# Performance work log

Hardware: AMD Instinct MI355X
Metric: run time of the kernel (lower is better)

The kernel has to match this reference:

```python
import jax, jax.numpy as jnp
import numpy as np

N_HEADS = 16
DIM = 1024
NEG_INF = -1e20  # neginf for fp32 per original module


def setup_inputs() -> dict:
    key = jax.random.key(0)
    ks = jax.random.split(key, 10)
    B, N, D = 2, 2048, DIM
    std = np.sqrt(2.0 / (D + D))  # xavier_normal for square weights
    inp = {
        "query": jax.random.normal(ks[0], (B, N, D), dtype=jnp.float32),
        "mask": jax.random.randint(ks[1], (B, N), 0, 2, dtype=jnp.int32),
        "wq": jax.random.normal(ks[2], (D, D), dtype=jnp.float32) * std,
        "bq": jnp.zeros((D,), dtype=jnp.float32),
        "wk": jax.random.normal(ks[3], (D, D), dtype=jnp.float32) * std,
        "bk": jnp.zeros((D,), dtype=jnp.float32),
        "wv": jax.random.normal(ks[4], (D, D), dtype=jnp.float32) * std,
        "bv": jnp.zeros((D,), dtype=jnp.float32),
        "wo": jax.random.normal(ks[5], (D, D), dtype=jnp.float32) * std,
        "bo": jnp.zeros((D,), dtype=jnp.float32),
    }
    return inp


def reference(query, mask, wq, bq, wk, bk, wv, bv, wo, bo):
    B, N, D = query.shape
    H = N_HEADS
    dh = D // H
    scale = jnp.asarray(np.sqrt(dh), dtype=query.dtype)

    def heads(x):  # [B,N,D] -> [B,H,N,dh]
        return x.reshape(B, N, H, dh).transpose(0, 2, 1, 3)

    q = heads(query @ wq.T + bq) / scale
    k = heads(query @ wk.T + bk)
    v = heads(query @ wv.T + bv)

    # [B,H,Nq,Nk] scaled dot-product scores, masked where mask==0
    dot_prod = jnp.einsum("bhqd,bhkd->bhqk", q, k)
    dot_prod = jnp.where(mask[:, None, None, :] == 0, NEG_INF, dot_prod)

    attn = jax.nn.softmax(dot_prod.astype(jnp.float32), axis=-1).astype(query.dtype)
    # dropout p=0 -> identity
    ctx = jnp.einsum("bhqk,bhkd->bhqd", attn, v)
    ctx = ctx.transpose(0, 2, 1, 3).reshape(B, N, D)
    out = ctx @ wo.T + bo
    # original returns dot_prod as [B*H, Nq, Nk]
    return out, dot_prod.reshape(B * H, N, N)
```

## Files before the change

### kernel.cpp

```cpp
#include <hip/hip_runtime.h>

typedef unsigned short u16;
typedef __attribute__((ext_vector_type(8))) __bf16 bf16x8;
typedef __attribute__((ext_vector_type(4))) float f32x4;

#define MFMA(a, b, c) __builtin_amdgcn_mfma_f32_16x16x32_bf16((a), (b), (c), 0, 0, 0)

__device__ __forceinline__ u16 f2bf(float f) {
  union { float f; unsigned u; } v; v.f = f;
  unsigned r = v.u + 0x7fffu + ((v.u >> 16) & 1u);
  return (u16)(r >> 16);
}

__device__ __forceinline__ void gld16(const u16* g, u16* l) {
  __builtin_amdgcn_global_load_lds(
      (const __attribute__((address_space(1))) unsigned int*)(g),
      (__attribute__((address_space(3))) unsigned int*)(l), 16, 0, 0);
}

__global__ __launch_bounds__(256) void k_cast(
    const float* __restrict__ query, const float* __restrict__ wq,
    const float* __restrict__ wk, const float* __restrict__ wv,
    const float* __restrict__ wo, u16* __restrict__ dst)
{
  size_t i = ((size_t)blockIdx.x * 256 + threadIdx.x) * 8;
  const float* src; size_t off; float sc = 1.0f;
  if (i < 4194304u)      { src = query; off = i; }
  else if (i < 5242880u) { src = wq; off = i - 4194304u; sc = 0.125f; }
  else if (i < 6291456u) { src = wk; off = i - 5242880u; }
  else if (i < 7340032u) { src = wv; off = i - 6291456u; }
  else                   { src = wo; off = i - 7340032u; }
  float4 a = *(const float4*)(src + off);
  float4 b = *(const float4*)(src + off + 4);
  alignas(16) u16 r[8] = { f2bf(a.x*sc), f2bf(a.y*sc), f2bf(a.z*sc), f2bf(a.w*sc),
                           f2bf(b.x*sc), f2bf(b.y*sc), f2bf(b.z*sc), f2bf(b.w*sc) };
  *(int4*)(dst + i) = *(int4*)r;
}

__global__ __launch_bounds__(256) void k_gemm_qkv(
    const u16* __restrict__ Ab, const u16* __restrict__ Wb,
    const float* __restrict__ bq, const float* __restrict__ bk, const float* __restrict__ bv,
    u16* __restrict__ Qh, u16* __restrict__ Kh, u16* __restrict__ Vh)
{
  const int fb = blockIdx.x;
  const int sb = (fb & 7) * 96 + (fb >> 3);
  const int n0 = (sb % 24) * 128;
  const int m0 = (sb / 24) * 128;
  const int tid = threadIdx.x;
  const int w = tid >> 6, lane = tid & 63, g = lane >> 4, l15 = lane & 15;
  const int wm = w >> 1, wn = w & 1;
  __shared__ alignas(16) u16 As[128 * 32];
  __shared__ alignas(16) u16 Bs[128 * 32];
  f32x4 acc[4][4] = {};
  for (int k0 = 0; k0 < 1024; k0 += 32) {
    __syncthreads();
#pragma unroll
    for (int t = 0; t < 2; ++t) {
      int i = t * 256 + tid;
      int row = i >> 2, ch = i & 3, sch = ch ^ (row & 3);
      gld16(Ab + (size_t)(m0 + row) * 1024 + k0 + sch * 8, As + i * 8);
    }
#pragma unroll
    for (int t = 0; t < 2; ++t) {
      int i = t * 256 + tid;
      int row = i >> 2, ch = i & 3, sch = ch ^ (row & 3);
      gld16(Wb + (size_t)(n0 + row) * 1024 + k0 + sch * 8, Bs + i * 8);
    }
    __syncthreads();
    bf16x8 af[4], bfr[4];
#pragma unroll
    for (int i = 0; i < 4; ++i) {
      int row = wm * 64 + i * 16 + l15;
      af[i] = *(const bf16x8*)(As + (row * 4 + (g ^ (row & 3))) * 8);
    }
#pragma unroll
    for (int j = 0; j < 4; ++j) {
      int row = wn * 64 + j * 16 + l15;
      bfr[j] = *(const bf16x8*)(Bs + (row * 4 + (g ^ (row & 3))) * 8);
    }
#pragma unroll
    for (int i = 0; i < 4; ++i)
#pragma unroll
      for (int j = 0; j < 4; ++j)
        acc[i][j] = MFMA(af[i], bfr[j], acc[i][j]);
  }
  const int proj = n0 >> 10;
  const float* bias = (proj == 0) ? bq : (proj == 1) ? bk : bv;
  const float bsc = (proj == 0) ? 0.125f : 1.0f;
  u16* dst = (proj == 0) ? Qh : (proj == 1) ? Kh : Vh;
#pragma unroll
  for (int i = 0; i < 4; ++i)
#pragma unroll
    for (int j = 0; j < 4; ++j)
#pragma unroll
      for (int jj = 0; jj < 4; ++jj) {
        int mr = m0 + wm * 64 + i * 16 + g * 4 + jj;
        int c  = n0 + wn * 64 + j * 16 + l15;
        int d = c & 1023, h = d >> 6, d64 = d & 63;
        int b = mr >> 11, n = mr & 2047;
        float v = acc[i][j][jj] + bias[d] * bsc;
        dst[((size_t)((b << 4) | h) * 2048 + n) * 64 + d64] = f2bf(v);
      }
}

__global__ __launch_bounds__(256) void k_gemm_out(
    const u16* __restrict__ Ab, const u16* __restrict__ Wb,
    const float* __restrict__ bo, float* __restrict__ out)
{
  const int fb = blockIdx.x;
  const int sb = (fb & 7) * 32 + (fb >> 3);
  const int n0 = (sb & 7) * 128;
  const int m0 = (sb >> 3) * 128;
  const int tid = threadIdx.x;
  const int w = tid >> 6, lane = tid & 63, g = lane >> 4, l15 = lane & 15;
  const int wm = w >> 1, wn = w & 1;
  __shared__ alignas(16) u16 As[128 * 32];
  __shared__ alignas(16) u16 Bs[128 * 32];
  f32x4 acc[4][4] = {};
  for (int k0 = 0; k0 < 1024; k0 += 32) {
    __syncthreads();
#pragma unroll
    for (int t = 0; t < 2; ++t) {
      int i = t * 256 + tid;
      int row = i >> 2, ch = i & 3, sch = ch ^ (row & 3);
      gld16(Ab + (size_t)(m0 + row) * 1024 + k0 + sch * 8, As + i * 8);
    }
#pragma unroll
    for (int t = 0; t < 2; ++t) {
      int i = t * 256 + tid;
      int row = i >> 2, ch = i & 3, sch = ch ^ (row & 3);
      gld16(Wb + (size_t)(n0 + row) * 1024 + k0 + sch * 8, Bs + i * 8);
    }
    __syncthreads();
    bf16x8 af[4], bfr[4];
#pragma unroll
    for (int i = 0; i < 4; ++i) {
      int row = wm * 64 + i * 16 + l15;
      af[i] = *(const bf16x8*)(As + (row * 4 + (g ^ (row & 3))) * 8);
    }
#pragma unroll
    for (int j = 0; j < 4; ++j) {
      int row = wn * 64 + j * 16 + l15;
      bfr[j] = *(const bf16x8*)(Bs + (row * 4 + (g ^ (row & 3))) * 8);
    }
#pragma unroll
    for (int i = 0; i < 4; ++i)
#pragma unroll
      for (int j = 0; j < 4; ++j)
        acc[i][j] = MFMA(af[i], bfr[j], acc[i][j]);
  }
#pragma unroll
  for (int i = 0; i < 4; ++i)
#pragma unroll
    for (int j = 0; j < 4; ++j)
#pragma unroll
      for (int jj = 0; jj < 4; ++jj) {
        int mr = m0 + wm * 64 + i * 16 + g * 4 + jj;
        int c  = n0 + wn * 64 + j * 16 + l15;
        out[(size_t)mr * 1024 + c] = acc[i][j][jj] + bo[c];
      }
}

__global__ __launch_bounds__(256) void k_transpose_v(
    const u16* __restrict__ Vh, u16* __restrict__ Vt)
{
  const int n0 = blockIdx.x * 64;
  const int bh = blockIdx.y;
  const int tid = threadIdx.x;
  __shared__ alignas(16) u16 t[64][72];
  const u16* src = Vh + ((size_t)bh * 2048 + n0) * 64;
#pragma unroll
  for (int it = 0; it < 2; ++it) {
    int i = it * 256 + tid;
    int row = i >> 3, c = (i & 7) * 8;
    *(int4*)(&t[row][c]) = *(const int4*)(src + i * 8);
  }
  __syncthreads();
#pragma unroll
  for (int it = 0; it < 2; ++it) {
    int i = it * 256 + tid;
    int d = i >> 3, nn = (i & 7) * 8;
    alignas(16) u16 tmp[8];
#pragma unroll
    for (int e = 0; e < 8; ++e) tmp[e] = t[nn + e][d];
    *(int4*)(Vt + ((size_t)bh * 64 + d) * 2048 + n0 + nn) = *(int4*)tmp;
  }
}

__global__ __launch_bounds__(256) void k_attn(
    const u16* __restrict__ Qh, const u16* __restrict__ Kh, const u16* __restrict__ Vt,
    const int* __restrict__ mask, float* __restrict__ dout, u16* __restrict__ ctx)
{
  const int fb = blockIdx.x;
  const int sb = (fb & 7) * 128 + (fb >> 3);
  const int qt = sb & 31;
  const int bh = sb >> 5;
  const int b  = bh >> 4;
  const int tid = threadIdx.x;
  const int w = tid >> 6, lane = tid & 63, g = lane >> 4, l15 = lane & 15;
  __shared__ alignas(16) u16 Ks[128 * 64];
  __shared__ alignas(16) u16 Vs[64 * 128];
  __shared__ alignas(16) u16 Ps[4][16 * 136];

  const u16* Qrow = Qh + ((size_t)bh * 2048 + qt * 64 + w * 16 + l15) * 64;
  bf16x8 qf[2];
  qf[0] = *(const bf16x8*)(Qrow + g * 8);
  qf[1] = *(const bf16x8*)(Qrow + 32 + g * 8);

  float m[4] = {-3e38f, -3e38f, -3e38f, -3e38f};
  float l[4] = {0.f, 0.f, 0.f, 0.f};
  f32x4 O[4] = {};
  const int* maskb = mask + b * 2048;
  float* Sbase = dout + 4194304 + (size_t)bh * 4194304
               + (size_t)(qt * 64 + w * 16 + g * 4) * 2048 + l15;

  for (int kt = 0; kt < 16; ++kt) {
    __syncthreads();
    const u16* Kg = Kh + ((size_t)bh * 2048 + kt * 128) * 64;
#pragma unroll
    for (int it = 0; it < 4; ++it) {
      int i = it * 256 + tid;
      int row = i >> 3, ch = i & 7, sch = ch ^ (row & 7);
      gld16(Kg + row * 64 + sch * 8, Ks + i * 8);
    }
    const u16* Vg = Vt + (size_t)bh * 131072 + kt * 128;
#pragma unroll
    for (int it = 0; it < 4; ++it) {
      int i = it * 256 + tid;
      int row = i >> 4, ch = i & 15, sch = ch ^ (row & 15);
      gld16(Vg + (size_t)row * 2048 + sch * 8, Vs + i * 8);
    }
    int mk[8];
#pragma unroll
    for (int f = 0; f < 8; ++f) mk[f] = maskb[kt * 128 + f * 16 + l15];
    __syncthreads();

    f32x4 s[8];
#pragma unroll
    for (int f = 0; f < 8; ++f) {
      int row = f * 16 + l15;
      bf16x8 kf0 = *(const bf16x8*)(Ks + (row * 8 + ((0 + g) ^ (row & 7))) * 8);
      bf16x8 kf1 = *(const bf16x8*)(Ks + (row * 8 + ((4 + g) ^ (row & 7))) * 8);
      f32x4 t = {};
      t = MFMA(qf[0], kf0, t);
      t = MFMA(qf[1], kf1, t);
      s[f] = t;
    }

    float fb8[8];
#pragma unroll
    for (int f = 0; f < 8; ++f) fb8[f] = (mk[f] != 0) ? 0.f : -1e20f;

    float mloc[4] = {-3e38f, -3e38f, -3e38f, -3e38f};
#pragma unroll
    for (int jj = 0; jj < 4; ++jj)
#pragma unroll
      for (int f = 0; f < 8; ++f) {
        float sv = s[f][jj] + fb8[f];
        s[f][jj] = sv;
        __builtin_nontemporal_store(sv, &Sbase[(size_t)jj * 2048 + kt * 128 + f * 16]);
        mloc[jj] = fmaxf(mloc[jj], sv);
      }
#pragma unroll
    for (int d = 1; d < 16; d <<= 1)
#pragma unroll
      for (int jj = 0; jj < 4; ++jj)
        mloc[jj] = fmaxf(mloc[jj], __shfl_xor(mloc[jj], d, 64));

    float corr[4];
#pragma unroll
    for (int jj = 0; jj < 4; ++jj) {
      float mn = fmaxf(m[jj], mloc[jj]);
      corr[jj] = __expf(m[jj] - mn);
      m[jj] = mn;
    }
    float psum[4] = {0.f, 0.f, 0.f, 0.f};
#pragma unroll
    for (int f = 0; f < 8; ++f)
#pragma unroll
      for (int jj = 0; jj < 4; ++jj) {
        float p = __expf(s[f][jj] - m[jj]);
        psum[jj] += p;
        Ps[w][(g * 4 + jj) * 136 + f * 16 + l15] = f2bf(p);
      }
#pragma unroll
    for (int d = 1; d < 16; d <<= 1)
#pragma unroll
      for (int jj = 0; jj < 4; ++jj)
        psum[jj] += __shfl_xor(psum[jj], d, 64);
#pragma unroll
    for (int jj = 0; jj < 4; ++jj) l[jj] = l[jj] * corr[jj] + psum[jj];
#pragma unroll
    for (int fd = 0; fd < 4; ++fd)
#pragma unroll
      for (int jj = 0; jj < 4; ++jj) O[fd][jj] *= corr[jj];

#pragma unroll
    for (int fk = 0; fk < 4; ++fk) {
      bf16x8 pa = *(const bf16x8*)(&Ps[w][l15 * 136 + fk * 32 + g * 8]);
#pragma unroll
      for (int fd = 0; fd < 4; ++fd) {
        int row = fd * 16 + l15;
        bf16x8 bv = *(const bf16x8*)(Vs + (row * 16 + ((fk * 4 + g) ^ (row & 15))) * 8);
        O[fd] = MFMA(pa, bv, O[fd]);
      }
    }
  }
  float inv[4];
#pragma unroll
  for (int jj = 0; jj < 4; ++jj) inv[jj] = 1.0f / l[jj];
  const int h = bh & 15;
#pragma unroll
  for (int fd = 0; fd < 4; ++fd)
#pragma unroll
    for (int jj = 0; jj < 4; ++jj) {
      int n = qt * 64 + w * 16 + g * 4 + jj;
      int c = h * 64 + fd * 16 + l15;
      ctx[((size_t)(b * 2048 + n)) * 1024 + c] = f2bf(O[fd][jj] * inv[jj]);
    }
}

extern "C" void kernel_launch(void* const* d_in, const int* in_sizes, int n_in,
                              void* d_out, int out_size, void* d_ws, size_t ws_size,
                              hipStream_t stream)
{
  const float* query = (const float*)d_in[0];
  const int*   mask  = (const int*)d_in[1];
  const float* wq = (const float*)d_in[2];
  const float* bq = (const float*)d_in[3];
  const float* wk = (const float*)d_in[4];
  const float* bk = (const float*)d_in[5];
  const float* wv = (const float*)d_in[6];
  const float* bv = (const float*)d_in[7];
  const float* wo = (const float*)d_in[8];
  const float* bo = (const float*)d_in[9];
  float* out = (float*)d_out;

  u16* ws   = (u16*)d_ws;
  u16* Ab   = ws;
  u16* Wqkv = ws + 4194304;
  u16* Wo   = ws + 7340032;
  u16* Qh   = ws + 8388608;
  u16* Kh   = ws + 12582912;
  u16* Vh   = ws + 16777216;
  u16* Vt   = ws + 20971520;
  u16* ctx  = ws + 25165824;

  k_cast<<<4096, 256, 0, stream>>>(query, wq, wk, wv, wo, ws);
  k_gemm_qkv<<<768, 256, 0, stream>>>(Ab, Wqkv, bq, bk, bv, Qh, Kh, Vh);
  k_transpose_v<<<dim3(32, 32), 256, 0, stream>>>(Vh, Vt);
  k_attn<<<1024, 256, 0, stream>>>(Qh, Kh, Vt, mask, out, ctx);
  k_gemm_out<<<256, 256, 0, stream>>>(ctx, Wo, bo, out);
}
```

Before: 211.2 us.

## Transpose MFMA operands so each lane owns one query row in attention

Swaps the A/B operands of both attention MFMAs so the accumulator layout gives each lane a single query row and four consecutive key columns. Softmax state then collapses to one scalar per lane, and cross-lane reductions shrink to two shuffles. This also enables 16-byte vectorized score stores to the dot_prod output, int4 mask loads, packed bf16 writes of P and ctx, and a clamp on exp arguments. The main target is the large fp32 score write, which now uses wide stores instead of scattered scalar ones.

```diff
diff --git a/kernel.cpp b/kernel.cpp
--- a/kernel.cpp
+++ b/kernel.cpp
@@ -1,6 +1,7 @@
 #include <hip/hip_runtime.h>
 
 typedef unsigned short u16;
+typedef unsigned int u32;
 typedef __attribute__((ext_vector_type(8))) __bf16 bf16x8;
 typedef __attribute__((ext_vector_type(4))) float f32x4;
 
@@ -10,6 +11,10 @@
   union { float f; unsigned u; } v; v.f = f;
   unsigned r = v.u + 0x7fffu + ((v.u >> 16) & 1u);
   return (u16)(r >> 16);
+}
+
+__device__ __forceinline__ u32 pk2bf(float lo, float hi) {
+  return (u32)f2bf(lo) | ((u32)f2bf(hi) << 16);
 }
 
 __device__ __forceinline__ void gld16(const u16* g, u16* l) {
@@ -203,16 +208,14 @@
   __shared__ alignas(16) u16 Ps[4][16 * 136];
 
   const u16* Qrow = Qh + ((size_t)bh * 2048 + qt * 64 + w * 16 + l15) * 64;
-  bf16x8 qf[2];
-  qf[0] = *(const bf16x8*)(Qrow + g * 8);
-  qf[1] = *(const bf16x8*)(Qrow + 32 + g * 8);
-
-  float m[4] = {-3e38f, -3e38f, -3e38f, -3e38f};
-  float l[4] = {0.f, 0.f, 0.f, 0.f};
+  bf16x8 qf0 = *(const bf16x8*)(Qrow + g * 8);
+  bf16x8 qf1 = *(const bf16x8*)(Qrow + 32 + g * 8);
+
+  float m = -3e38f, l = 0.f;
   f32x4 O[4] = {};
   const int* maskb = mask + b * 2048;
-  float* Sbase = dout + 4194304 + (size_t)bh * 4194304
-               + (size_t)(qt * 64 + w * 16 + g * 4) * 2048 + l15;
+  float* Srow = dout + 4194304 + (size_t)bh * 4194304
+              + (size_t)(qt * 64 + w * 16 + l15) * 2048;
 
   for (int kt = 0; kt < 16; ++kt) {
     __syncthreads();
@@ -230,9 +233,6 @@
       int row = i >> 4, ch = i & 15, sch = ch ^ (row & 15);
       gld16(Vg + (size_t)row * 2048 + sch * 8, Vs + i * 8);
     }
-    int mk[8];
-#pragma unroll
-    for (int f = 0; f < 8; ++f) mk[f] = maskb[kt * 128 + f * 16 + l15];
     __syncthreads();
 
     f32x4 s[8];
@@ -242,58 +242,48 @@
       bf16x8 kf0 = *(const bf16x8*)(Ks + (row * 8 + ((0 + g) ^ (row & 7))) * 8);
       bf16x8 kf1 = *(const bf16x8*)(Ks + (row * 8 + ((4 + g) ^ (row & 7))) * 8);
       f32x4 t = {};
-      t = MFMA(qf[0], kf0, t);
-      t = MFMA(qf[1], kf1, t);
+      t = MFMA(kf0, qf0, t);
+      t = MFMA(kf1, qf1, t);
       s[f] = t;
     }
 
-    float fb8[8];
-#pragma unroll
-    for (int f = 0; f < 8; ++f) fb8[f] = (mk[f] != 0) ? 0.f : -1e20f;
-
-    float mloc[4] = {-3e38f, -3e38f, -3e38f, -3e38f};
-#pragma unroll
-    for (int jj = 0; jj < 4; ++jj)
-#pragma unroll
-      for (int f = 0; f < 8; ++f) {
-        float sv = s[f][jj] + fb8[f];
-        s[f][jj] = sv;
-        __builtin_nontemporal_store(sv, &Sbase[(size_t)jj * 2048 + kt * 128 + f * 16]);
-        mloc[jj] = fmaxf(mloc[jj], sv);
-      }
-#pragma unroll
-    for (int d = 1; d < 16; d <<= 1)
-#pragma unroll
-      for (int jj = 0; jj < 4; ++jj)
-        mloc[jj] = fmaxf(mloc[jj], __shfl_xor(mloc[jj], d, 64));
-
-    float corr[4];
-#pragma unroll
-    for (int jj = 0; jj < 4; ++jj) {
-      float mn = fmaxf(m[jj], mloc[jj]);
-      corr[jj] = __expf(m[jj] - mn);
-      m[jj] = mn;
-    }
-    float psum[4] = {0.f, 0.f, 0.f, 0.f};
-#pragma unroll
-    for (int f = 0; f < 8; ++f)
-#pragma unroll
-      for (int jj = 0; jj < 4; ++jj) {
-        float p = __expf(s[f][jj] - m[jj]);
-        psum[jj] += p;
-        Ps[w][(g * 4 + jj) * 136 + f * 16 + l15] = f2bf(p);
-      }
-#pragma unroll
-    for (int d = 1; d < 16; d <<= 1)
-#pragma unroll
-      for (int jj = 0; jj < 4; ++jj)
-        psum[jj] += __shfl_xor(psum[jj], d, 64);
-#pragma unroll
-    for (int jj = 0; jj < 4; ++jj) l[jj] = l[jj] * corr[jj] + psum[jj];
+    float mloc = -3e38f;
+#pragma unroll
+    for (int f = 0; f < 8; ++f) {
+      int4 mk = *(const int4*)(maskb + kt * 128 + f * 16 + g * 4);
+      s[f][0] += (mk.x != 0) ? 0.f : -1e20f;
+      s[f][1] += (mk.y != 0) ? 0.f : -1e20f;
+      s[f][2] += (mk.z != 0) ? 0.f : -1e20f;
+      s[f][3] += (mk.w != 0) ? 0.f : -1e20f;
+      __builtin_nontemporal_store(s[f],
+          (f32x4*)(Srow + kt * 128 + f * 16 + g * 4));
+      mloc = fmaxf(mloc, fmaxf(fmaxf(s[f][0], s[f][1]), fmaxf(s[f][2], s[f][3])));
+    }
+    mloc = fmaxf(mloc, __shfl_xor(mloc, 16, 64));
+    mloc = fmaxf(mloc, __shfl_xor(mloc, 32, 64));
+
+    float mn = fmaxf(m, mloc);
+    float corr = __expf(m - mn);
+    m = mn;
+
+    float ps = 0.f;
+#pragma unroll
+    for (int f = 0; f < 8; ++f) {
+      float p0 = __expf(fminf(s[f][0] - mn, 0.f));
+      float p1 = __expf(fminf(s[f][1] - mn, 0.f));
+      float p2 = __expf(fminf(s[f][2] - mn, 0.f));
+      float p3 = __expf(fminf(s[f][3] - mn, 0.f));
+      ps += (p0 + p1) + (p2 + p3);
+      uint2 pk = { pk2bf(p0, p1), pk2bf(p2, p3) };
+      *(uint2*)(&Ps[w][l15 * 136 + f * 16 + g * 4]) = pk;
+    }
+    ps += __shfl_xor(ps, 16, 64);
+    ps += __shfl_xor(ps, 32, 64);
+    l = l * corr + ps;
 #pragma unroll
     for (int fd = 0; fd < 4; ++fd)
 #pragma unroll
-      for (int jj = 0; jj < 4; ++jj) O[fd][jj] *= corr[jj];
+      for (int jj = 0; jj < 4; ++jj) O[fd][jj] *= corr;
 
 #pragma unroll
     for (int fk = 0; fk < 4; ++fk) {
@@ -302,22 +292,19 @@
       for (int fd = 0; fd < 4; ++fd) {
         int row = fd * 16 + l15;
         bf16x8 bv = *(const bf16x8*)(Vs + (row * 16 + ((fk * 4 + g) ^ (row & 15))) * 8);
-        O[fd] = MFMA(pa, bv, O[fd]);
+        O[fd] = MFMA(bv, pa, O[fd]);
       }
     }
   }
-  float inv[4];
-#pragma unroll
-  for (int jj = 0; jj < 4; ++jj) inv[jj] = 1.0f / l[jj];
+  float inv = 1.0f / l;
   const int h = bh & 15;
-#pragma unroll
-  for (int fd = 0; fd < 4; ++fd)
-#pragma unroll
-    for (int jj = 0; jj < 4; ++jj) {
-      int n = qt * 64 + w * 16 + g * 4 + jj;
-      int c = h * 64 + fd * 16 + l15;
-      ctx[((size_t)(b * 2048 + n)) * 1024 + c] = f2bf(O[fd][jj] * inv[jj]);
-    }
+  const size_t nbase = ((size_t)(b * 2048 + qt * 64 + w * 16 + l15)) * 1024 + h * 64;
+#pragma unroll
+  for (int fd = 0; fd < 4; ++fd) {
+    uint2 pk = { pk2bf(O[fd][0] * inv, O[fd][1] * inv),
+                 pk2bf(O[fd][2] * inv, O[fd][3] * inv) };
+    *(uint2*)(ctx + nbase + fd * 16 + g * 4) = pk;
+  }
 }
 
 extern "C" void kernel_launch(void* const* d_in, const int* in_sizes, int n_in,
```

After: 276.8 us. 1.31x slower.

## Double-buffer LDS tiles in GEMMs and attention with async prefetch

Applied to the files above, without the earlier changes.

Both GEMM kernels now use two LDS buffers and issue the global-to-LDS loads for the next K slice before computing on the current one, with a single barrier per iteration. The attention kernel shrinks its key tile from 128 to 64 and double-buffers K and V the same way, prefetching the next tile while the current tile's scores, softmax and PV products are computed. The aim is to hide global load latency behind MFMA work, at the cost of more LDS, twice as many loop iterations in attention, and more reliance on the load/compute ordering being correct without a wait before reads.

```diff
diff --git a/kernel.cpp b/kernel.cpp
--- a/kernel.cpp
+++ b/kernel.cpp
@@ -1,6 +1,7 @@
 #include <hip/hip_runtime.h>
 
 typedef unsigned short u16;
+typedef unsigned int u32;
 typedef __attribute__((ext_vector_type(8))) __bf16 bf16x8;
 typedef __attribute__((ext_vector_type(4))) float f32x4;
 
@@ -49,40 +50,48 @@
   const int tid = threadIdx.x;
   const int w = tid >> 6, lane = tid & 63, g = lane >> 4, l15 = lane & 15;
   const int wm = w >> 1, wn = w & 1;
-  __shared__ alignas(16) u16 As[128 * 32];
-  __shared__ alignas(16) u16 Bs[128 * 32];
-  f32x4 acc[4][4] = {};
-  for (int k0 = 0; k0 < 1024; k0 += 32) {
-    __syncthreads();
+  __shared__ alignas(16) u16 As[2][128 * 32];
+  __shared__ alignas(16) u16 Bs[2][128 * 32];
+
+  auto stage = [&](int buf, int k0) {
 #pragma unroll
     for (int t = 0; t < 2; ++t) {
       int i = t * 256 + tid;
       int row = i >> 2, ch = i & 3, sch = ch ^ (row & 3);
-      gld16(Ab + (size_t)(m0 + row) * 1024 + k0 + sch * 8, As + i * 8);
+      gld16(Ab + (size_t)(m0 + row) * 1024 + k0 + sch * 8, &As[buf][i * 8]);
     }
 #pragma unroll
     for (int t = 0; t < 2; ++t) {
       int i = t * 256 + tid;
       int row = i >> 2, ch = i & 3, sch = ch ^ (row & 3);
-      gld16(Wb + (size_t)(n0 + row) * 1024 + k0 + sch * 8, Bs + i * 8);
-    }
-    __syncthreads();
+      gld16(Wb + (size_t)(n0 + row) * 1024 + k0 + sch * 8, &Bs[buf][i * 8]);
+    }
+  };
+
+  f32x4 acc[4][4] = {};
+  stage(0, 0);
+  __syncthreads();
+  int cur = 0;
+  for (int k0 = 0; k0 < 1024; k0 += 32) {
+    if (k0 + 32 < 1024) stage(cur ^ 1, k0 + 32);
     bf16x8 af[4], bfr[4];
 #pragma unroll
     for (int i = 0; i < 4; ++i) {
       int row = wm * 64 + i * 16 + l15;
-      af[i] = *(const bf16x8*)(As + (row * 4 + (g ^ (row & 3))) * 8);
+      af[i] = *(const bf16x8*)(&As[cur][(row * 4 + (g ^ (row & 3))) * 8]);
     }
 #pragma unroll
     for (int j = 0; j < 4; ++j) {
       int row = wn * 64 + j * 16 + l15;
-      bfr[j] = *(const bf16x8*)(Bs + (row * 4 + (g ^ (row & 3))) * 8);
+      bfr[j] = *(const bf16x8*)(&Bs[cur][(row * 4 + (g ^ (row & 3))) * 8]);
     }
 #pragma unroll
     for (int i = 0; i < 4; ++i)
 #pragma unroll
       for (int j = 0; j < 4; ++j)
         acc[i][j] = MFMA(af[i], bfr[j], acc[i][j]);
+    __syncthreads();
+    cur ^= 1;
   }
   const int proj = n0 >> 10;
   const float* bias = (proj == 0) ? bq : (proj == 1) ? bk : bv;
@@ -114,40 +123,48 @@
   const int tid = threadIdx.x;
   const int w = tid >> 6, lane = tid & 63, g = lane >> 4, l15 = lane & 15;
   const int wm = w >> 1, wn = w & 1;
-  __shared__ alignas(16) u16 As[128 * 32];
-  __shared__ alignas(16) u16 Bs[128 * 32];
-  f32x4 acc[4][4] = {};
-  for (int k0 = 0; k0 < 1024; k0 += 32) {
-    __syncthreads();
+  __shared__ alignas(16) u16 As[2][128 * 32];
+  __shared__ alignas(16) u16 Bs[2][128 * 32];
+
+  auto stage = [&](int buf, int k0) {
 #pragma unroll
     for (int t = 0; t < 2; ++t) {
       int i = t * 256 + tid;
       int row = i >> 2, ch = i & 3, sch = ch ^ (row & 3);
-      gld16(Ab + (size_t)(m0 + row) * 1024 + k0 + sch * 8, As + i * 8);
+      gld16(Ab + (size_t)(m0 + row) * 1024 + k0 + sch * 8, &As[buf][i * 8]);
     }
 #pragma unroll
     for (int t = 0; t < 2; ++t) {
       int i = t * 256 + tid;
       int row = i >> 2, ch = i & 3, sch = ch ^ (row & 3);
-      gld16(Wb + (size_t)(n0 + row) * 1024 + k0 + sch * 8, Bs + i * 8);
-    }
-    __syncthreads();
+      gld16(Wb + (size_t)(n0 + row) * 1024 + k0 + sch * 8, &Bs[buf][i * 8]);
+    }
+  };
+
+  f32x4 acc[4][4] = {};
+  stage(0, 0);
+  __syncthreads();
+  int cur = 0;
+  for (int k0 = 0; k0 < 1024; k0 += 32) {
+    if (k0 + 32 < 1024) stage(cur ^ 1, k0 + 32);
     bf16x8 af[4], bfr[4];
 #pragma unroll
     for (int i = 0; i < 4; ++i) {
       int row = wm * 64 + i * 16 + l15;
-      af[i] = *(const bf16x8*)(As + (row * 4 + (g ^ (row & 3))) * 8);
+      af[i] = *(const bf16x8*)(&As[cur][(row * 4 + (g ^ (row & 3))) * 8]);
     }
 #pragma unroll
     for (int j = 0; j < 4; ++j) {
       int row = wn * 64 + j * 16 + l15;
-      bfr[j] = *(const bf16x8*)(Bs + (row * 4 + (g ^ (row & 3))) * 8);
+      bfr[j] = *(const bf16x8*)(&Bs[cur][(row * 4 + (g ^ (row & 3))) * 8]);
     }
 #pragma unroll
     for (int i = 0; i < 4; ++i)
 #pragma unroll
       for (int j = 0; j < 4; ++j)
         acc[i][j] = MFMA(af[i], bfr[j], acc[i][j]);
+    __syncthreads();
+    cur ^= 1;
   }
 #pragma unroll
   for (int i = 0; i < 4; ++i)
@@ -198,14 +215,36 @@
   const int b  = bh >> 4;
   const int tid = threadIdx.x;
   const int w = tid >> 6, lane = tid & 63, g = lane >> 4, l15 = lane & 15;
-  __shared__ alignas(16) u16 Ks[128 * 64];
-  __shared__ alignas(16) u16 Vs[64 * 128];
-  __shared__ alignas(16) u16 Ps[4][16 * 136];
+  __shared__ alignas(16) u16 Ks[2][64 * 64];
+  __shared__ alignas(16) u16 Vs[2][64 * 64];
+  __shared__ alignas(16) u16 Ps[4][16 * 72];
 
   const u16* Qrow = Qh + ((size_t)bh * 2048 + qt * 64 + w * 16 + l15) * 64;
-  bf16x8 qf[2];
-  qf[0] = *(const bf16x8*)(Qrow + g * 8);
-  qf[1] = *(const bf16x8*)(Qrow + 32 + g * 8);
+  bf16x8 qf0 = *(const bf16x8*)(Qrow + g * 8);
+  bf16x8 qf1 = *(const bf16x8*)(Qrow + 32 + g * 8);
+
+  const u16* Kb = Kh + (size_t)bh * 131072;
+  const u16* Vb = Vt + (size_t)bh * 131072;
+
+  auto stageK = [&](int buf, int kt) {
+#pragma unroll
+    for (int it = 0; it < 2; ++it) {
+      int i = it * 256 + tid;
+      int row = i >> 3, ch = i & 7, sch = ch ^ (row & 7);
+      gld16(Kb + (size_t)(kt * 64 + row) * 64 + sch * 8, &Ks[buf][i * 8]);
+    }
+  };
+  auto stageV = [&](int buf, int kt) {
+#pragma unroll
+    for (int it = 0; it < 2; ++it) {
+      int i = it * 256 + tid;
+      int row = i >> 3, ch = i & 7, sch = ch ^ (row & 7);
+      gld16(Vb + (size_t)row * 2048 + kt * 64 + sch * 8, &Vs[buf][i * 8]);
+    }
+  };
+
+  stageK(0, 0); stageV(0, 0);
+  __syncthreads();
 
   float m[4] = {-3e38f, -3e38f, -3e38f, -3e38f};
   float l[4] = {0.f, 0.f, 0.f, 0.f};
@@ -214,51 +253,38 @@
   float* Sbase = dout + 4194304 + (size_t)bh * 4194304
                + (size_t)(qt * 64 + w * 16 + g * 4) * 2048 + l15;
 
-  for (int kt = 0; kt < 16; ++kt) {
-    __syncthreads();
-    const u16* Kg = Kh + ((size_t)bh * 2048 + kt * 128) * 64;
-#pragma unroll
-    for (int it = 0; it < 4; ++it) {
-      int i = it * 256 + tid;
-      int row = i >> 3, ch = i & 7, sch = ch ^ (row & 7);
-      gld16(Kg + row * 64 + sch * 8, Ks + i * 8);
-    }
-    const u16* Vg = Vt + (size_t)bh * 131072 + kt * 128;
-#pragma unroll
-    for (int it = 0; it < 4; ++it) {
-      int i = it * 256 + tid;
-      int row = i >> 4, ch = i & 15, sch = ch ^ (row & 15);
-      gld16(Vg + (size_t)row * 2048 + sch * 8, Vs + i * 8);
-    }
-    int mk[8];
-#pragma unroll
-    for (int f = 0; f < 8; ++f) mk[f] = maskb[kt * 128 + f * 16 + l15];
-    __syncthreads();
-
-    f32x4 s[8];
-#pragma unroll
-    for (int f = 0; f < 8; ++f) {
+  int cur = 0;
+  for (int kt = 0; kt < 32; ++kt) {
+    if (kt + 1 < 32) { stageK(cur ^ 1, kt + 1); stageV(cur ^ 1, kt + 1); }
+
+    int mk[4];
+#pragma unroll
+    for (int f = 0; f < 4; ++f) mk[f] = maskb[kt * 64 + f * 16 + l15];
+
+    f32x4 s[4];
+#pragma unroll
+    for (int f = 0; f < 4; ++f) {
       int row = f * 16 + l15;
-      bf16x8 kf0 = *(const bf16x8*)(Ks + (row * 8 + ((0 + g) ^ (row & 7))) * 8);
-      bf16x8 kf1 = *(const bf16x8*)(Ks + (row * 8 + ((4 + g) ^ (row & 7))) * 8);
+      bf16x8 kf0 = *(const bf16x8*)(&Ks[cur][(row * 8 + ((0 + g) ^ (row & 7))) * 8]);
+      bf16x8 kf1 = *(const bf16x8*)(&Ks[cur][(row * 8 + ((4 + g) ^ (row & 7))) * 8]);
       f32x4 t = {};
-      t = MFMA(qf[0], kf0, t);
-      t = MFMA(qf[1], kf1, t);
+      t = MFMA(qf0, kf0, t);
+      t = MFMA(qf1, kf1, t);
       s[f] = t;
     }
 
-    float fb8[8];
-#pragma unroll
-    for (int f = 0; f < 8; ++f) fb8[f] = (mk[f] != 0) ? 0.f : -1e20f;
+    float fb4[4];
+#pragma unroll
+    for (int f = 0; f < 4; ++f) fb4[f] = (mk[f] != 0) ? 0.f : -1e20f;
 
     float mloc[4] = {-3e38f, -3e38f, -3e38f, -3e38f};
 #pragma unroll
     for (int jj = 0; jj < 4; ++jj)
 #pragma unroll
-      for (int f = 0; f < 8; ++f) {
-        float sv = s[f][jj] + fb8[f];
+      for (int f = 0; f < 4; ++f) {
+        float sv = s[f][jj] + fb4[f];
         s[f][jj] = sv;
-        __builtin_nontemporal_store(sv, &Sbase[(size_t)jj * 2048 + kt * 128 + f * 16]);
+        __builtin_nontemporal_store(sv, &Sbase[(size_t)jj * 2048 + kt * 64 + f * 16]);
         mloc[jj] = fmaxf(mloc[jj], sv);
       }
 #pragma unroll
@@ -276,12 +302,12 @@
     }
     float psum[4] = {0.f, 0.f, 0.f, 0.f};
 #pragma unroll
-    for (int f = 0; f < 8; ++f)
+    for (int f = 0; f < 4; ++f)
 #pragma unroll
       for (int jj = 0; jj < 4; ++jj) {
         float p = __expf(s[f][jj] - m[jj]);
         psum[jj] += p;
-        Ps[w][(g * 4 + jj) * 136 + f * 16 + l15] = f2bf(p);
+        Ps[w][(g * 4 + jj) * 72 + f * 16 + l15] = f2bf(p);
       }
 #pragma unroll
     for (int d = 1; d < 16; d <<= 1)
@@ -296,15 +322,17 @@
       for (int jj = 0; jj < 4; ++jj) O[fd][jj] *= corr[jj];
 
 #pragma unroll
-    for (int fk = 0; fk < 4; ++fk) {
-      bf16x8 pa = *(const bf16x8*)(&Ps[w][l15 * 136 + fk * 32 + g * 8]);
+    for (int fk = 0; fk < 2; ++fk) {
+      bf16x8 pa = *(const bf16x8*)(&Ps[w][l15 * 72 + fk * 32 + g * 8]);
 #pragma unroll
       for (int fd = 0; fd < 4; ++fd) {
         int row = fd * 16 + l15;
-        bf16x8 bv = *(const bf16x8*)(Vs + (row * 16 + ((fk * 4 + g) ^ (row & 15))) * 8);
+        bf16x8 bv = *(const bf16x8*)(&Vs[cur][(row * 8 + ((fk * 4 + g) ^ (row & 7))) * 8]);
         O[fd] = MFMA(pa, bv, O[fd]);
       }
     }
+    __syncthreads();
+    cur ^= 1;
   }
   float inv[4];
 #pragma unroll
```

New measurement: 233.0 us. +10.3%, slower.
